# Performance work log

Hardware: AMD Instinct MI355X
Metric: run time of the kernel (lower is better)

## Reference

```python
import jax, jax.numpy as jnp
from jax import lax
import numpy as np

IN, G, H, L = 128, 5, 512, 256   # input_size, n_genres, hidden_dim, latent_dim
E = 2 * H                         # encoder_hidden_dim (bidirectional)
B, T = 128, 256
SLOPE = 0.01                      # torch LeakyReLU default


def _gru(xt, h, Wih, Whh, bih, bhh):
    # torch.nn.GRUCell: gates ordered r, z, n
    gi = xt @ Wih.T + bih         # [B, 3H]
    gh = h @ Whh.T + bhh          # [B, 3H]
    ir, iz, inn = jnp.split(gi, 3, axis=-1)
    hr, hz, hn = jnp.split(gh, 3, axis=-1)
    r = jax.nn.sigmoid(ir + hr)
    z = jax.nn.sigmoid(iz + hz)
    n = jnp.tanh(inn + r * hn)
    return (1.0 - z) * n + z * h


def _leaky(v):
    return jnp.where(v >= 0, v, SLOPE * v)


def setup_inputs() -> dict:
    key = jax.random.key(0)
    ks = jax.random.split(key, 32)
    it = iter(range(32))

    def p(shape, fan_in):
        s = 1.0 / np.sqrt(fan_in)
        return jax.random.uniform(ks[next(it)], shape, jnp.float32, -s, s)

    inp = {
        "x": jax.random.normal(ks[next(it)], (B, T, IN + G), jnp.float32),
        "latent_genre_vec": jax.random.uniform(ks[next(it)], (B, G), jnp.float32),
        "eps": jax.random.normal(ks[next(it)], (B, L - G), jnp.float32),
    }
    # forward encoder GRUCell (input IN+G -> H)
    inp["Wih_e"] = p((3 * H, IN + G), H); inp["Whh_e"] = p((3 * H, H), H)
    inp["bih_e"] = p((3 * H,), H);        inp["bhh_e"] = p((3 * H,), H)
    # backward encoder GRUCell
    inp["Wih_be"] = p((3 * H, IN + G), H); inp["Whh_be"] = p((3 * H, H), H)
    inp["bih_be"] = p((3 * H,), H);        inp["bhh_be"] = p((3 * H,), H)
    # decoder GRUCell (input IN -> H)
    inp["Wih_d"] = p((3 * H, IN), H); inp["Whh_d"] = p((3 * H, H), H)
    inp["bih_d"] = p((3 * H,), H);    inp["bhh_d"] = p((3 * H,), H)
    # fc_mu: [Linear(E,E)+LeakyReLU, Linear(E, L-G)]
    inp["W_mu0"] = p((E, E), E); inp["b_mu0"] = p((E,), E)
    inp["W_mu1"] = p((L - G, E), E); inp["b_mu1"] = p((L - G,), E)
    # fc_logvar
    inp["W_lv0"] = p((E, E), E); inp["b_lv0"] = p((E,), E)
    inp["W_lv1"] = p((L - G, E), E); inp["b_lv1"] = p((L - G,), E)
    # fc_latent: [Linear(L,L)+LeakyReLU, Linear(L, H)]
    inp["W_lat0"] = p((L, L), L); inp["b_lat0"] = p((L,), L)
    inp["W_lat1"] = p((H, L), L); inp["b_lat1"] = p((H,), L)
    # fc_decoder final Linear(H, IN) (fc_decoder[0] is dead code in the original loop)
    inp["W_dec1"] = p((IN, H), H); inp["b_dec1"] = p((IN,), H)
    return inp


def reference(x, latent_genre_vec, eps,
              Wih_e, Whh_e, bih_e, bhh_e,
              Wih_be, Whh_be, bih_be, bhh_be,
              Wih_d, Whh_d, bih_d, bhh_d,
              W_mu0, b_mu0, W_mu1, b_mu1,
              W_lv0, b_lv0, W_lv1, b_lv1,
              W_lat0, b_lat0, W_lat1, b_lat1,
              W_dec1, b_dec1):
    b = x.shape[0]
    xs = jnp.swapaxes(x, 0, 1)  # [T, B, IN+G]
    h0 = jnp.zeros((b, H), x.dtype)

    def enc_step(h, xt):
        return _gru(xt, h, Wih_e, Whh_e, bih_e, bhh_e), None

    def benc_step(h, xt):
        return _gru(xt, h, Wih_be, Whh_be, bih_be, bhh_be), None

    h_fwd, _ = lax.scan(enc_step, h0, xs)
    h_bwd, _ = lax.scan(benc_step, h0, xs, reverse=True)
    hidden = jnp.concatenate([h_fwd, h_bwd], axis=1)  # [B, 2H]

    mu = _leaky(hidden @ W_mu0.T + b_mu0) @ W_mu1.T + b_mu1        # [B, L-G]
    logvar = _leaky(hidden @ W_lv0.T + b_lv0) @ W_lv1.T + b_lv1    # [B, L-G]

    z = mu + jnp.exp(0.5 * logvar) * eps
    z = jnp.concatenate([z, latent_genre_vec], axis=1)             # [B, L]

    dec_h = _leaky(z @ W_lat0.T + b_lat0) @ W_lat1.T + b_lat1      # [B, H]

    note0 = x[:, 0, :IN]  # [B, IN]

    def dec_step(carry, _):
        h, note = carry
        h = _gru(note, h, Wih_d, Whh_d, bih_d, bhh_d)
        # faithful to original: final fc_decoder layer applied to hidden
        note = h @ W_dec1.T + b_dec1
        return (h, note), note

    _, notes = lax.scan(dec_step, (dec_h, note0), None, length=x.shape[1] - 1)
    output = jnp.concatenate([note0[:, None, :], jnp.swapaxes(notes, 0, 1)], axis=1)  # [B, T, IN]
    return output, mu, logvar
```

## Files before the change

### kernel.cpp

```cpp
#include <hip/hip_runtime.h>

#define B_ 128
#define T_ 256
#define IN_ 128
#define G_ 5
#define H_ 512
#define G3_ 1536
#define E_ 1024
#define L_ 256
#define LG_ 251
#define INPG_ 133

#define MU_OFF (B_*T_*IN_)
#define LV_OFF (MU_OFF + B_*LG_)

typedef __attribute__((ext_vector_type(8))) short bf16x8;
typedef __attribute__((ext_vector_type(4))) float f32x4;
typedef unsigned long long u64;

__device__ __forceinline__ float bf2f(unsigned short s) {
    return __uint_as_float(((unsigned)s) << 16);
}
__device__ __forceinline__ unsigned short f2bf(float f) {
    unsigned x = __float_as_uint(f);
    unsigned r = (x + 0x7fffu + ((x >> 16) & 1u)) >> 16;
    return (unsigned short)r;
}
__device__ __forceinline__ float sigf(float v) {
    return 1.f / (1.f + __expf(-v));
}
__device__ __forceinline__ int ld_flag(const int* p) {
    return __hip_atomic_load(p, __ATOMIC_RELAXED, __HIP_MEMORY_SCOPE_AGENT);
}
__device__ __forceinline__ void st_flag(int* p, int v) {
    __hip_atomic_store(p, v, __ATOMIC_RELAXED, __HIP_MEMORY_SCOPE_AGENT);
}
__device__ __forceinline__ u64 ld_h64(const void* p) {
    return __hip_atomic_load((const u64*)p, __ATOMIC_RELAXED, __HIP_MEMORY_SCOPE_AGENT);
}
__device__ __forceinline__ void st_h32(void* p, unsigned v) {
    __hip_atomic_store((unsigned*)p, v, __ATOMIC_RELAXED, __HIP_MEMORY_SCOPE_AGENT);
}


__global__ void xpad_k(const float* __restrict__ x, ushort* __restrict__ xb) {
    int id = blockIdx.x * 256 + threadIdx.x;
    if (id >= T_ * B_ * 160) return;
    int t = id / (B_ * 160);
    int rem = id - t * (B_ * 160);
    int b = rem / 160, c = rem - b * 160;
    float v = (c < INPG_) ? x[((size_t)b * T_ + t) * INPG_ + c] : 0.f;
    xb[id] = f2bf(v);
}

__global__ void pack_we(const float* __restrict__ Wih_f, const float* __restrict__ Whh_f,
                        const float* __restrict__ Wih_b, const float* __restrict__ Whh_b,
                        ushort* __restrict__ WE) {
    int id = blockIdx.x * 256 + threadIdx.x;
    int lane = id & 63;
    int rest = id >> 6;
    int ks = rest % 63;
    int cb = (rest / 63) & 31;
    int dir = rest / (63 * 32);
    if (dir >= 2) return;
    const float* Wih = dir ? Wih_b : Wih_f;
    const float* Whh = dir ? Whh_b : Whh_f;
    int n = lane & 15, kb = lane >> 4;
    int p, ksp;
    if (ks < 21)      { p = 0; ksp = ks; }
    else if (ks < 42) { p = 1; ksp = ks - 21; }
    else if (ks < 47) { p = 2; ksp = ks - 42; }
    else              { p = 3; ksp = ks - 47; }
    int j = cb * 16 + n;
    int row = (p == 0) ? j : (p == 1) ? 512 + j : 1024 + j;
    #pragma unroll
    for (int e = 0; e < 8; ++e) {
        int k = ksp * 32 + kb * 8 + e;
        float v;
        if (p == 3)      v = Whh[(size_t)row * 512 + k];
        else if (p == 2) v = (k < INPG_) ? Wih[(size_t)row * INPG_ + k] : 0.f;
        else v = (k < INPG_) ? Wih[(size_t)row * INPG_ + k]
               : (k < 160)   ? 0.f
               : Whh[(size_t)row * 512 + (k - 160)];
        WE[(size_t)id * 8 + e] = f2bf(v);
    }
}

__global__ void wfused_k(const float* __restrict__ Wih_d, const float* __restrict__ Wdec1,
                         float* __restrict__ Wf) {
    int id = blockIdx.x * 256 + threadIdx.x;
    if (id >= G3_ * H_) return;
    int r = id >> 9, c = id & 511;
    float s = 0.f;
    for (int m = 0; m < 128; ++m)
        s += Wih_d[(size_t)r * 128 + m] * Wdec1[(size_t)m * 512 + c];
    Wf[id] = s;
}

__global__ void bfi_k(const float* __restrict__ Wih_d, const float* __restrict__ b_dec1,
                      const float* __restrict__ bih_d, float* __restrict__ bfi) {
    int r = blockIdx.x * 256 + threadIdx.x;
    if (r >= G3_) return;
    float s = bih_d[r];
    for (int m = 0; m < 128; ++m)
        s += Wih_d[(size_t)r * 128 + m] * b_dec1[m];
    bfi[r] = s;
}

__global__ void pack_wd(const float* __restrict__ Wf, const float* __restrict__ Whh,
                        ushort* __restrict__ WD, int fused) {
    int id = blockIdx.x * 256 + threadIdx.x;
    int lane = id & 63;
    int rest = id >> 6;
    int ks = rest & 63;
    int cb = rest >> 6;
    if (cb >= 32) return;
    int p = ks >> 4, ksp = ks & 15;
    int n = lane & 15, kb = lane >> 4;
    int j = cb * 16 + n;
    int row = (p == 0) ? j : (p == 1) ? 512 + j : 1024 + j;
    #pragma unroll
    for (int e = 0; e < 8; ++e) {
        int k = ksp * 32 + kb * 8 + e;
        float v;
        if (p <= 1) v = fused ? (Wf[(size_t)row * 512 + k] + Whh[(size_t)row * 512 + k])
                              : Whh[(size_t)row * 512 + k];
        else if (p == 2) v = fused ? Wf[(size_t)row * 512 + k] : 0.f;
        else v = Whh[(size_t)row * 512 + k];
        WD[(size_t)id * 8 + e] = f2bf(v);
    }
}

__global__ void pack_wdec(const float* __restrict__ Wdec1, ushort* __restrict__ pk) {
    int id = blockIdx.x * 256 + threadIdx.x;
    if (id >= 8192) return;
    int lane = id & 63, ch = id >> 6;
    int nt = ch >> 4, ks = ch & 15;
    int n = nt * 16 + (lane & 15);
    int k0 = ks * 32 + (lane >> 4) * 8;
    #pragma unroll
    for (int e = 0; e < 8; ++e)
        pk[(size_t)id * 8 + e] = f2bf(Wdec1[(size_t)n * 512 + k0 + e]);
}

__global__ void zero_init(ushort* __restrict__ hb, int* __restrict__ ef,
                          int* __restrict__ df) {
    int id = blockIdx.x * 256 + threadIdx.x;
    if (id < 4 * 65536) hb[id] = 0;
    if (id < 4096) ef[id] = 0;
    if (id < 2048) df[id] = 0;
}

__global__ void note0_k2(const float* __restrict__ x, float* __restrict__ out,
                         float* __restrict__ note0f) {
    int id = blockIdx.x * 256 + threadIdx.x;
    if (id >= B_ * IN_) return;
    int b = id >> 7, n = id & 127;
    float v = x[((size_t)b * T_) * INPG_ + n];
    out[((size_t)b * T_) * IN_ + n] = v;
    note0f[(size_t)b * 128 + n] = v;
}

__global__ void cvt_h0(const float* __restrict__ src, ushort* __restrict__ dst) {
    int id = blockIdx.x * 256 + threadIdx.x;
    if (id < B_ * H_) dst[id] = f2bf(src[id]);
}

__global__ void tile_w(const float* __restrict__ W, ushort4* __restrict__ out,
                       int N, int K, int KC) {
    int id = blockIdx.x * 256 + threadIdx.x;
    if (id >= KC * N) return;
    int kc = id / N, n = id - kc * N;
    int k = kc * 4;
    ushort4 u;
    u.x = f2bf(k + 0 < K ? W[(size_t)n * K + k + 0] : 0.f);
    u.y = f2bf(k + 1 < K ? W[(size_t)n * K + k + 1] : 0.f);
    u.z = f2bf(k + 2 < K ? W[(size_t)n * K + k + 2] : 0.f);
    u.w = f2bf(k + 3 < K ? W[(size_t)n * K + k + 3] : 0.f);
    out[(size_t)kc * N + n] = u;
}

__global__ __launch_bounds__(256) void enc_persist(
    const ushort* __restrict__ xb16, const ushort* __restrict__ WE,
    ushort* __restrict__ hb,
    float* __restrict__ hidden,
    const float* __restrict__ bih_f, const float* __restrict__ bhh_f,
    const float* __restrict__ bih_b, const float* __restrict__ bhh_b,
    int* __restrict__ flags)
{
    __shared__ ushort As[32 * 680];
    __shared__ ushort Ws[63 * 512];
    __shared__ float gs[4][512];
    int bid = blockIdx.x;
    int dir = bid >> 7, bt = (bid >> 5) & 3, cb = bid & 31;
    int b0 = bt * 32;
    int tid = threadIdx.x;
    const float* bih = dir ? bih_b : bih_f;
    const float* bhh = dir ? bhh_b : bhh_f;

    {
        const ushort* src = WE + (size_t)((dir * 32 + cb) * 63) * 512;
        for (int c = tid; c < 4032; c += 256)
            *(uint4*)&Ws[c * 8] = *(const uint4*)&src[c * 8];
    }
    int bA = tid >> 3;
    int j0 = cb * 16 + 2 * (tid & 7), j1 = j0 + 1;
    float b_r0 = bih[j0] + bhh[j0],        b_r1 = bih[j1] + bhh[j1];
    float b_z0 = bih[512 + j0] + bhh[512 + j0], b_z1 = bih[512 + j1] + bhh[512 + j1];
    float b_in0 = bih[1024 + j0],          b_in1 = bih[1024 + j1];
    float b_hn0 = bhh[1024 + j0],          b_hn1 = bhh[1024 + j1];
    float hc0 = 0.f, hc1 = 0.f;

    int lane = tid & 63, wv = tid >> 6;
    int m = lane & 15, kb = lane >> 4;
    int nk  = (wv == 2) ? 5 : (wv == 3) ? 16 : 21;
    int ksb = (wv == 0) ? 0 : (wv == 1) ? 21 : (wv == 2) ? 42 : 47;
    int kcol0 = (wv == 3) ? 160 : 0;
    int ai0 = m * 680 + kcol0 + kb * 8;
    int ai1 = (16 + m) * 680 + kcol0 + kb * 8;
    const int* fpoll = &flags[((bid & ~31) + (lane & 31)) * 16];

    auto stage_x = [&](int t2) {
        int tt2 = dir ? (255 - t2) : t2;
        const ushort* xr2 = xb16 + (size_t)tt2 * (B_ * 160);
        #pragma unroll
        for (int i = 0; i < 3; ++i) {
            int c = tid + i * 256;
            if (c < 640) {
                int row = c / 20, off = c - row * 20;
                *(uint4*)((char*)As + row * 1360 + off * 16) =
                    *(const uint4*)(xr2 + (size_t)(b0 + row) * 160 + off * 8);
            }
        }
    };
    stage_x(0);

    for (int t = 0; t < T_; ++t) {
        int pp = t & 1;
        const ushort* hin = hb + (size_t)(pp * 2 + dir) * 65536;
        ushort* hout = hb + (size_t)((pp ^ 1) * 2 + dir) * 65536;
        if (t > 0) {
            if (wv == 0)
                while (!__all(ld_flag(fpoll) >= t)) __builtin_amdgcn_s_sleep(1);
            __syncthreads();
        }
        {
            u64 vb[16];
            #pragma unroll
            for (int i = 0; i < 16; ++i) {
                int c = tid + i * 256;
                int row = c >> 7, off = c & 127;
                vb[i] = ld_h64(hin + (size_t)(b0 + row) * 512 + off * 4);
            }
            #pragma unroll
            for (int i = 0; i < 16; ++i) {
                int c = tid + i * 256;
                int row = c >> 7, off = c & 127;
                *(u64*)((char*)As + row * 1360 + 320 + off * 8) = vb[i];
            }
        }
        __syncthreads();
        f32x4 acc0 = {0.f,0.f,0.f,0.f}, acc1 = {0.f,0.f,0.f,0.f};
        const ushort* Bp = &Ws[ksb * 512 + lane * 8];
        for (int ks = 0; ks < nk; ++ks) {
            bf16x8 bfr = *(const bf16x8*)(Bp + (size_t)ks * 512);
            bf16x8 a0 = *(const bf16x8*)&As[ai0 + ks * 32];
            bf16x8 a1 = *(const bf16x8*)&As[ai1 + ks * 32];
            acc0 = __builtin_amdgcn_mfma_f32_16x16x32_bf16(a0, bfr, acc0, 0, 0, 0);
            acc1 = __builtin_amdgcn_mfma_f32_16x16x32_bf16(a1, bfr, acc1, 0, 0, 0);
        }
        #pragma unroll
        for (int i = 0; i < 4; ++i) {
            gs[wv][(kb * 4 + i) * 16 + m] = acc0[i];
            gs[wv][(16 + kb * 4 + i) * 16 + m] = acc1[i];
        }
        __syncthreads();
        {
            int o0 = 2 * tid, o1 = o0 + 1;
            float r0 = sigf(gs[0][o0] + b_r0);
            float z0 = sigf(gs[1][o0] + b_z0);
            float n0 = tanhf(gs[2][o0] + b_in0 + r0 * (gs[3][o0] + b_hn0));
            hc0 = (1.f - z0) * n0 + z0 * hc0;
            float r1 = sigf(gs[0][o1] + b_r1);
            float z1 = sigf(gs[1][o1] + b_z1);
            float n1 = tanhf(gs[2][o1] + b_in1 + r1 * (gs[3][o1] + b_hn1));
            hc1 = (1.f - z1) * n1 + z1 * hc1;
            unsigned pkd = (unsigned)f2bf(hc0) | ((unsigned)f2bf(hc1) << 16);
            st_h32((char*)hout + ((size_t)(b0 + bA) * 512 + j0) * 2, pkd);
            if (t == 255) {
                float2 hv = {hc0, hc1};
                *(float2*)&hidden[(size_t)(b0 + bA) * 1024 + dir * 512 + j0] = hv;
            }
        }
        __syncthreads();
        if (t < 255) {
            if (tid == 0) st_flag(&flags[bid * 16], t + 1);
            stage_x(t + 1);
        }
    }
}

__global__ __launch_bounds__(256) void dec_persist(
    const ushort* __restrict__ hdec0, const ushort* __restrict__ WD2,
    const ushort* __restrict__ WD1, ushort* __restrict__ hist,
    const float* __restrict__ h0f, const float* __restrict__ bfi,
    const float* __restrict__ bhh, const float* __restrict__ gi0,
    int* __restrict__ flags)
{
    __shared__ ushort As[32 * 520];
    __shared__ ushort Ws[64 * 512];
    __shared__ float gs[4][512];
    int bid = blockIdx.x;
    int bt = bid >> 5, cb = bid & 31;
    int b0 = bt * 32, tid = threadIdx.x;
    {
        const ushort* src = WD2 + (size_t)(cb * 64) * 512;
        for (int c = tid; c < 4096; c += 256)
            *(uint4*)&Ws[c * 8] = *(const uint4*)&src[c * 8];
    }
    int bA = tid >> 3;
    int j0 = cb * 16 + 2 * (tid & 7), j1 = j0 + 1;
    float f_r0 = bfi[j0] + bhh[j0],             f_r1 = bfi[j1] + bhh[j1];
    float f_z0 = bfi[512 + j0] + bhh[512 + j0], f_z1 = bfi[512 + j1] + bhh[512 + j1];
    float f_in0 = bfi[1024 + j0],               f_in1 = bfi[1024 + j1];
    float f_hn0 = bhh[1024 + j0],               f_hn1 = bhh[1024 + j1];
    float bh_r0 = bhh[j0], bh_r1 = bhh[j1];
    float bh_z0 = bhh[512 + j0], bh_z1 = bhh[512 + j1];
    float hc0 = h0f[(size_t)(b0 + bA) * 512 + j0];
    float hc1 = h0f[(size_t)(b0 + bA) * 512 + j1];
    float g0r = gi0[(size_t)(b0 + bA) * G3_ + j0];
    float g1r = gi0[(size_t)(b0 + bA) * G3_ + j1];
    float g0z = gi0[(size_t)(b0 + bA) * G3_ + 512 + j0];
    float g1z = gi0[(size_t)(b0 + bA) * G3_ + 512 + j1];
    float g0n = gi0[(size_t)(b0 + bA) * G3_ + 1024 + j0];
    float g1n = gi0[(size_t)(b0 + bA) * G3_ + 1024 + j1];

    int lane = tid & 63, wv = tid >> 6;
    int m = lane & 15, kb = lane >> 4;
    int ai0 = m * 520 + kb * 8, ai1 = (16 + m) * 520 + kb * 8;
    const ushort* WD1s = WD1 + (size_t)(cb * 64 + wv * 16) * 512 + lane * 8;
    const int* fpoll = &flags[((bid & ~31) + (lane & 31)) * 16];

    for (int t = 1; t < T_; ++t) {
        if (t >= 2) {
            if (wv == 0)
                while (!__all(ld_flag(fpoll) >= t - 1)) __builtin_amdgcn_s_sleep(1);
            __syncthreads();
        }
        const ushort* hsrc = (t == 1) ? hdec0 : hist + (size_t)(t - 2) * 65536;
        {
            u64 vb[16];
            #pragma unroll
            for (int i = 0; i < 16; ++i) {
                int c = tid + i * 256;
                int row = c >> 7, off = c & 127;
                vb[i] = ld_h64(hsrc + (size_t)(b0 + row) * 512 + off * 4);
            }
            #pragma unroll
            for (int i = 0; i < 16; ++i) {
                int c = tid + i * 256;
                int row = c >> 7, off = c & 127;
                *(u64*)((char*)As + row * 1040 + off * 8) = vb[i];
            }
        }
        __syncthreads();
        f32x4 acc0 = {0.f,0.f,0.f,0.f}, acc1 = {0.f,0.f,0.f,0.f};
        if (t == 1) {
            if (wv != 2) {
                for (int ks = 0; ks < 16; ++ks) {
                    bf16x8 bfr = *(const bf16x8*)(WD1s + (size_t)ks * 512);
                    bf16x8 a0 = *(const bf16x8*)&As[ai0 + ks * 32];
                    bf16x8 a1 = *(const bf16x8*)&As[ai1 + ks * 32];
                    acc0 = __builtin_amdgcn_mfma_f32_16x16x32_bf16(a0, bfr, acc0, 0, 0, 0);
                    acc1 = __builtin_amdgcn_mfma_f32_16x16x32_bf16(a1, bfr, acc1, 0, 0, 0);
                }
            }
        } else {
            const ushort* Bp = &Ws[(wv * 16) * 512 + lane * 8];
            for (int ks = 0; ks < 16; ++ks) {
                bf16x8 bfr = *(const bf16x8*)(Bp + (size_t)ks * 512);
                bf16x8 a0 = *(const bf16x8*)&As[ai0 + ks * 32];
                bf16x8 a1 = *(const bf16x8*)&As[ai1 + ks * 32];
                acc0 = __builtin_amdgcn_mfma_f32_16x16x32_bf16(a0, bfr, acc0, 0, 0, 0);
                acc1 = __builtin_amdgcn_mfma_f32_16x16x32_bf16(a1, bfr, acc1, 0, 0, 0);
            }
        }
        #pragma unroll
        for (int i = 0; i < 4; ++i) {
            gs[wv][(kb * 4 + i) * 16 + m] = acc0[i];
            gs[wv][(16 + kb * 4 + i) * 16 + m] = acc1[i];
        }
        __syncthreads();
        {
            int o0 = 2 * tid, o1 = o0 + 1;
            float r0, z0, n0, r1, z1, n1;
            if (t == 1) {
                r0 = sigf(gs[0][o0] + g0r + bh_r0);
                z0 = sigf(gs[1][o0] + g0z + bh_z0);
                n0 = tanhf(gs[2][o0] + g0n + r0 * (gs[3][o0] + f_hn0));
                r1 = sigf(gs[0][o1] + g1r + bh_r1);
                z1 = sigf(gs[1][o1] + g1z + bh_z1);
                n1 = tanhf(gs[2][o1] + g1n + r1 * (gs[3][o1] + f_hn1));
            } else {
                r0 = sigf(gs[0][o0] + f_r0);
                z0 = sigf(gs[1][o0] + f_z0);
                n0 = tanhf(gs[2][o0] + f_in0 + r0 * (gs[3][o0] + f_hn0));
                r1 = sigf(gs[0][o1] + f_r1);
                z1 = sigf(gs[1][o1] + f_z1);
                n1 = tanhf(gs[2][o1] + f_in1 + r1 * (gs[3][o1] + f_hn1));
            }
            hc0 = (1.f - z0) * n0 + z0 * hc0;
            hc1 = (1.f - z1) * n1 + z1 * hc1;
            unsigned pkd = (unsigned)f2bf(hc0) | ((unsigned)f2bf(hc1) << 16);
            st_h32((char*)(hist + (size_t)(t - 1) * 65536) +
                   ((size_t)(b0 + bA) * 512 + j0) * 2, pkd);
        }
        __syncthreads();
        if (t < 255 && tid == 0) st_flag(&flags[bid * 16], t);
    }
}

__global__ __launch_bounds__(256) void notes_mfma(
    const ushort* __restrict__ hist, const ushort* __restrict__ pk,
    const float* __restrict__ bd, float* __restrict__ out)
{
    __shared__ ushort hs[32 * 520];
    int m0 = blockIdx.x * 32;
    int tid = threadIdx.x;
    #pragma unroll
    for (int i = 0; i < 8; ++i) {
        int c = tid + i * 256;
        int row = c >> 6, off = c & 63;
        *(uint4*)((char*)hs + row * 1040 + off * 16) =
            *(const uint4*)(hist + (size_t)(m0 + row) * 512 + off * 8);
    }
    __syncthreads();
    int lane = tid & 63, wv = tid >> 6;
    int m = lane & 15, kb = lane >> 4;
    int nt0 = wv * 2;
    f32x4 acc00 = {0.f,0.f,0.f,0.f}, acc01 = {0.f,0.f,0.f,0.f};
    f32x4 acc10 = {0.f,0.f,0.f,0.f}, acc11 = {0.f,0.f,0.f,0.f};
    for (int ks = 0; ks < 16; ++ks) {
        bf16x8 a0 = *(const bf16x8*)&hs[m * 520 + ks * 32 + kb * 8];
        bf16x8 a1 = *(const bf16x8*)&hs[(16 + m) * 520 + ks * 32 + kb * 8];
        bf16x8 bf0 = *(const bf16x8*)&pk[(size_t)((nt0 * 16 + ks) * 64 + lane) * 8];
        bf16x8 bf1 = *(const bf16x8*)&pk[(size_t)(((nt0 + 1) * 16 + ks) * 64 + lane) * 8];
        acc00 = __builtin_amdgcn_mfma_f32_16x16x32_bf16(a0, bf0, acc00, 0, 0, 0);
        acc01 = __builtin_amdgcn_mfma_f32_16x16x32_bf16(a0, bf1, acc01, 0, 0, 0);
        acc10 = __builtin_amdgcn_mfma_f32_16x16x32_bf16(a1, bf0, acc10, 0, 0, 0);
        acc11 = __builtin_amdgcn_mfma_f32_16x16x32_bf16(a1, bf1, acc11, 0, 0, 0);
    }
    int n0 = nt0 * 16 + (lane & 15), n1 = (nt0 + 1) * 16 + (lane & 15);
    #pragma unroll
    for (int i = 0; i < 4; ++i) {
        int r0 = m0 + kb * 4 + i;
        int r1 = r0 + 16;
        int t0 = r0 >> 7, b0r = r0 & 127;
        int t1 = r1 >> 7, b1r = r1 & 127;
        out[((size_t)b0r * T_ + (t0 + 1)) * IN_ + n0] = acc00[i] + bd[n0];
        out[((size_t)b0r * T_ + (t0 + 1)) * IN_ + n1] = acc01[i] + bd[n1];
        out[((size_t)b1r * T_ + (t1 + 1)) * IN_ + n0] = acc10[i] + bd[n0];
        out[((size_t)b1r * T_ + (t1 + 1)) * IN_ + n1] = acc11[i] + bd[n1];
    }
}

__global__ __launch_bounds__(256) void gemm_t4(
    const float* __restrict__ A, const ushort4* __restrict__ Wt,
    const float* __restrict__ bias, float* __restrict__ C,
    int M, int N, int K, int act)
{
    int nb = blockIdx.x, mb = blockIdx.y;
    int tid = threadIdx.x;
    int n = nb * 64 + (tid & 63);
    int mq = tid >> 6;
    int m0 = mb * 32;
    __shared__ float Asm[32][36];
    float acc[8];
    #pragma unroll
    for (int i = 0; i < 8; ++i) acc[i] = 0.f;
    for (int k0 = 0; k0 < K; k0 += 32) {
        int r = tid >> 3, c = (tid & 7) << 2;
        float4 v = *(const float4*)&A[(size_t)(m0 + r) * K + k0 + c];
        Asm[r][c] = v.x; Asm[r][c+1] = v.y; Asm[r][c+2] = v.z; Asm[r][c+3] = v.w;
        __syncthreads();
        #pragma unroll
        for (int kc = 0; kc < 8; ++kc) {
            float w0 = 0.f, w1 = 0.f, w2 = 0.f, w3 = 0.f;
            if (n < N) {
                ushort4 u = Wt[(size_t)((k0 >> 2) + kc) * N + n];
                w0 = bf2f(u.x); w1 = bf2f(u.y); w2 = bf2f(u.z); w3 = bf2f(u.w);
            }
            #pragma unroll
            for (int i = 0; i < 8; ++i) {
                int mm = mq * 8 + i;
                acc[i] += Asm[mm][kc*4+0]*w0 + Asm[mm][kc*4+1]*w1
                        + Asm[mm][kc*4+2]*w2 + Asm[mm][kc*4+3]*w3;
            }
        }
        __syncthreads();
    }
    if (n < N) {
        #pragma unroll
        for (int i = 0; i < 8; ++i) {
            int mm = m0 + mq * 8 + i;
            float v = acc[i] + bias[n];
            if (act == 1) v = (v >= 0.f) ? v : 0.01f * v;
            C[(size_t)mm * N + n] = v;
        }
    }
}

__global__ void z_k(const float* __restrict__ out, const float* __restrict__ eps,
                    const float* __restrict__ genre, float* __restrict__ zc) {
    int id = blockIdx.x * 256 + threadIdx.x;
    if (id >= B_ * L_) return;
    int b = id >> 8, c = id & 255;
    float v;
    if (c < LG_) {
        float mu = out[MU_OFF + (size_t)b * LG_ + c];
        float lv = out[LV_OFF + (size_t)b * LG_ + c];
        v = mu + expf(0.5f * lv) * eps[(size_t)b * LG_ + c];
    } else {
        v = genre[(size_t)b * G_ + (c - LG_)];
    }
    zc[id] = v;
}

extern "C" void kernel_launch(void* const* d_in, const int* in_sizes, int n_in,
                              void* d_out, int out_size, void* d_ws, size_t ws_size,
                              hipStream_t stream) {
    (void)in_sizes; (void)n_in; (void)out_size; (void)ws_size;
    const float* x      = (const float*)d_in[0];
    const float* genre  = (const float*)d_in[1];
    const float* eps    = (const float*)d_in[2];
    const float* Wih_e  = (const float*)d_in[3];
    const float* Whh_e  = (const float*)d_in[4];
    const float* bih_e  = (const float*)d_in[5];
    const float* bhh_e  = (const float*)d_in[6];
    const float* Wih_be = (const float*)d_in[7];
    const float* Whh_be = (const float*)d_in[8];
    const float* bih_be = (const float*)d_in[9];
    const float* bhh_be = (const float*)d_in[10];
    const float* Wih_d  = (const float*)d_in[11];
    const float* Whh_d  = (const float*)d_in[12];
    const float* bih_d  = (const float*)d_in[13];
    const float* bhh_d  = (const float*)d_in[14];
    const float* W_mu0  = (const float*)d_in[15];
    const float* b_mu0  = (const float*)d_in[16];
    const float* W_mu1  = (const float*)d_in[17];
    const float* b_mu1  = (const float*)d_in[18];
    const float* W_lv0  = (const float*)d_in[19];
    const float* b_lv0  = (const float*)d_in[20];
    const float* W_lv1  = (const float*)d_in[21];
    const float* b_lv1  = (const float*)d_in[22];
    const float* W_lat0 = (const float*)d_in[23];
    const float* b_lat0 = (const float*)d_in[24];
    const float* W_lat1 = (const float*)d_in[25];
    const float* b_lat1 = (const float*)d_in[26];
    const float* W_dec1 = (const float*)d_in[27];
    const float* b_dec1 = (const float*)d_in[28];
    float* out = (float*)d_out;

    char* ws = (char*)d_ws;
    size_t off = 0;
    auto alloc = [&](size_t bytes) -> char* {
        char* p = ws + off;
        off = (off + bytes + 255) & ~(size_t)255;
        return p;
    };
    ushort* xb16  = (ushort*)alloc((size_t)T_ * B_ * 160 * 2);
    ushort* WE    = (ushort*)alloc((size_t)2 * 32 * 63 * 512 * 2);
    ushort* WD2   = (ushort*)alloc((size_t)32 * 64 * 512 * 2);
    ushort* WD1   = (ushort*)alloc((size_t)32 * 64 * 512 * 2);
    float*  Wf    = (float*)alloc((size_t)G3_ * H_ * 4);
    float*  bfi   = (float*)alloc(G3_ * 4);
    ushort* hb_e  = (ushort*)alloc((size_t)4 * 65536 * 2);
    ushort* hist  = (ushort*)alloc((size_t)255 * 65536 * 2);
    ushort* hdec0 = (ushort*)alloc((size_t)65536 * 2);
    ushort* pkdec = (ushort*)alloc((size_t)8192 * 8 * 2);
    int*    eflag = (int*)alloc((size_t)4096 * 4);
    int*    dflag = (int*)alloc((size_t)2048 * 4);
    float*  note0f= (float*)alloc((size_t)B_ * 128 * 4);
    float*  gi0   = (float*)alloc((size_t)B_ * G3_ * 4);
    float*  hidden= (float*)alloc((size_t)B_ * E_ * 4);
    float*  t0buf = (float*)alloc((size_t)B_ * E_ * 4);
    float*  t1buf = (float*)alloc((size_t)B_ * E_ * 4);
    float*  zcbuf = (float*)alloc((size_t)B_ * L_ * 4);
    float*  t2buf = (float*)alloc((size_t)B_ * L_ * 4);
    float*  t3buf = (float*)alloc((size_t)B_ * H_ * 4);

    ushort4* T_Wmu0  = (ushort4*)alloc((size_t)256 * E_ * 8);
    ushort4* T_Wmu1  = (ushort4*)alloc((size_t)256 * LG_ * 8);
    ushort4* T_Wlv0  = (ushort4*)alloc((size_t)256 * E_ * 8);
    ushort4* T_Wlv1  = (ushort4*)alloc((size_t)256 * LG_ * 8);
    ushort4* T_Wlat0 = (ushort4*)alloc((size_t)64 * L_ * 8);
    ushort4* T_Wlat1 = (ushort4*)alloc((size_t)64 * H_ * 8);
    ushort4* T_Wihd  = (ushort4*)alloc((size_t)32 * G3_ * 8);

    xpad_k<<<(T_ * B_ * 160 + 255) / 256, 256, 0, stream>>>(x, xb16);
    pack_we<<<1008, 256, 0, stream>>>(Wih_e, Whh_e, Wih_be, Whh_be, WE);
    wfused_k<<<(G3_ * H_ + 255) / 256, 256, 0, stream>>>(Wih_d, W_dec1, Wf);
    bfi_k<<<6, 256, 0, stream>>>(Wih_d, b_dec1, bih_d, bfi);
    pack_wd<<<512, 256, 0, stream>>>(Wf, Whh_d, WD2, 1);
    pack_wd<<<512, 256, 0, stream>>>(Wf, Whh_d, WD1, 0);
    pack_wdec<<<32, 256, 0, stream>>>(W_dec1, pkdec);
    zero_init<<<1024, 256, 0, stream>>>(hb_e, eflag, dflag);
    note0_k2<<<(B_ * IN_ + 255) / 256, 256, 0, stream>>>(x, out, note0f);

    auto tile = [&](const float* W, ushort4* dst, int N, int K) {
        int KC = (K + 3) / 4;
        tile_w<<<(KC * N + 255) / 256, 256, 0, stream>>>(W, dst, N, K, KC);
    };
    tile(W_mu0,  T_Wmu0,  E_,  E_);
    tile(W_mu1,  T_Wmu1,  LG_, E_);
    tile(W_lv0,  T_Wlv0,  E_,  E_);
    tile(W_lv1,  T_Wlv1,  LG_, E_);
    tile(W_lat0, T_Wlat0, L_,  L_);
    tile(W_lat1, T_Wlat1, H_,  L_);
    tile(Wih_d,  T_Wihd,  G3_, IN_);

    enc_persist<<<256, 256, 0, stream>>>(xb16, WE, hb_e, hidden,
                                         bih_e, bhh_e, bih_be, bhh_be, eflag);

    {
        dim3 g1(16, 4), g2(4, 4), g3(4, 4), g4(8, 4), g5(24, 4);
        gemm_t4<<<g1, 256, 0, stream>>>(hidden, T_Wmu0, b_mu0, t0buf, B_, E_, E_, 1);
        gemm_t4<<<g2, 256, 0, stream>>>(t0buf, T_Wmu1, b_mu1, out + MU_OFF, B_, LG_, E_, 0);
        gemm_t4<<<g1, 256, 0, stream>>>(hidden, T_Wlv0, b_lv0, t1buf, B_, E_, E_, 1);
        gemm_t4<<<g2, 256, 0, stream>>>(t1buf, T_Wlv1, b_lv1, out + LV_OFF, B_, LG_, E_, 0);
        z_k<<<(B_ * L_ + 255) / 256, 256, 0, stream>>>(out, eps, genre, zcbuf);
        gemm_t4<<<g3, 256, 0, stream>>>(zcbuf, T_Wlat0, b_lat0, t2buf, B_, L_, L_, 1);
        gemm_t4<<<g4, 256, 0, stream>>>(t2buf, T_Wlat1, b_lat1, t3buf, B_, H_, L_, 0);
        gemm_t4<<<g5, 256, 0, stream>>>(note0f, T_Wihd, bih_d, gi0, B_, G3_, IN_, 0);
    }
    cvt_h0<<<(B_ * H_ + 255) / 256, 256, 0, stream>>>(t3buf, hdec0);

    dec_persist<<<128, 256, 0, stream>>>(hdec0, WD2, WD1, hist, t3buf,
                                         bfi, bhh_d, gi0, dflag);

    notes_mfma<<<1020, 256, 0, stream>>>(hist, pkdec, b_dec1, out);
}
```

Baseline: 2.303 ms.

## Keep GRU weights in registers and compute all gates per wave in persistent RNN kernels

The encoder and decoder persistent kernels now run 128 threads per block, with each wave holding its slice of the r, z and n gate weights in VGPRs instead of LDS. Each wave computes all four gate accumulators for 16 batch rows, which removes the shared-memory gate exchange and two block barriers per timestep. Readiness flags are now per wave (two per block, polled as one 64-bit load), and hidden state is stored as 16-bit elements. Fast rcp-based sigmoid and tanh are also added. The risks are heavy register pressure from about 63 bf16x8 weight vectors per thread, and the use of approximate transcendentals.

```diff
diff --git a/kernel.cpp b/kernel.cpp
--- a/kernel.cpp
+++ b/kernel.cpp
@@ -27,7 +27,12 @@
     return (unsigned short)r;
 }
 __device__ __forceinline__ float sigf(float v) {
-    return 1.f / (1.f + __expf(-v));
+    return __builtin_amdgcn_rcpf(1.f + __expf(-v));
+}
+__device__ __forceinline__ float ftanh(float x) {
+    x = fminf(15.f, fmaxf(-15.f, x));
+    float e = __expf(2.f * x);
+    return (e - 1.f) * __builtin_amdgcn_rcpf(e + 1.f);
 }
 __device__ __forceinline__ int ld_flag(const int* p) {
     return __hip_atomic_load(p, __ATOMIC_RELAXED, __HIP_MEMORY_SCOPE_AGENT);
@@ -38,8 +43,11 @@
 __device__ __forceinline__ u64 ld_h64(const void* p) {
     return __hip_atomic_load((const u64*)p, __ATOMIC_RELAXED, __HIP_MEMORY_SCOPE_AGENT);
 }
-__device__ __forceinline__ void st_h32(void* p, unsigned v) {
-    __hip_atomic_store((unsigned*)p, v, __ATOMIC_RELAXED, __HIP_MEMORY_SCOPE_AGENT);
+__device__ __forceinline__ u64 ld_f64(const void* p) {
+    return __hip_atomic_load((const u64*)p, __ATOMIC_RELAXED, __HIP_MEMORY_SCOPE_AGENT);
+}
+__device__ __forceinline__ void st_h16(ushort* p, ushort v) {
+    __hip_atomic_store(p, v, __ATOMIC_RELAXED, __HIP_MEMORY_SCOPE_AGENT);
 }
 
 
@@ -143,10 +151,8 @@
         pk[(size_t)id * 8 + e] = f2bf(Wdec1[(size_t)n * 512 + k0 + e]);
 }
 
-__global__ void zero_init(ushort* __restrict__ hb, int* __restrict__ ef,
-                          int* __restrict__ df) {
-    int id = blockIdx.x * 256 + threadIdx.x;
-    if (id < 4 * 65536) hb[id] = 0;
+__global__ void zero_init(int* __restrict__ ef, int* __restrict__ df) {
+    int id = blockIdx.x * 256 + threadIdx.x;
     if (id < 4096) ef[id] = 0;
     if (id < 2048) df[id] = 0;
 }
@@ -180,7 +186,9 @@
     out[(size_t)kc * N + n] = u;
 }
 
-__global__ __launch_bounds__(256) void enc_persist(
+#define MFMA16(a, b, c) __builtin_amdgcn_mfma_f32_16x16x32_bf16((a), (b), (c), 0, 0, 0)
+
+__global__ __launch_bounds__(128) void enc_persist(
     const ushort* __restrict__ xb16, const ushort* __restrict__ WE,
     ushort* __restrict__ hb,
     float* __restrict__ hidden,
@@ -188,235 +196,236 @@
     const float* __restrict__ bih_b, const float* __restrict__ bhh_b,
     int* __restrict__ flags)
 {
-    __shared__ ushort As[32 * 680];
-    __shared__ ushort Ws[63 * 512];
-    __shared__ float gs[4][512];
+    __shared__ ushort As[52000];
     int bid = blockIdx.x;
     int dir = bid >> 7, bt = (bid >> 5) & 3, cb = bid & 31;
+    int gb = dir * 4 + bt;
     int b0 = bt * 32;
     int tid = threadIdx.x;
+    int lane = tid & 63, wv = tid >> 6;
     const float* bih = dir ? bih_b : bih_f;
     const float* bhh = dir ? bhh_b : bhh_f;
 
+    int m = lane & 15, kb = lane >> 4;
+    int j = cb * 16 + m;
+    int rowbase = wv * 16;
+    int rb = b0 + rowbase + ((lane >> 4) << 2);
+
+    bf16x8 wR[21], wZ[21], wNx[5], wNh[16];
     {
-        const ushort* src = WE + (size_t)((dir * 32 + cb) * 63) * 512;
-        for (int c = tid; c < 4032; c += 256)
-            *(uint4*)&Ws[c * 8] = *(const uint4*)&src[c * 8];
-    }
-    int bA = tid >> 3;
-    int j0 = cb * 16 + 2 * (tid & 7), j1 = j0 + 1;
-    float b_r0 = bih[j0] + bhh[j0],        b_r1 = bih[j1] + bhh[j1];
-    float b_z0 = bih[512 + j0] + bhh[512 + j0], b_z1 = bih[512 + j1] + bhh[512 + j1];
-    float b_in0 = bih[1024 + j0],          b_in1 = bih[1024 + j1];
-    float b_hn0 = bhh[1024 + j0],          b_hn1 = bhh[1024 + j1];
-    float hc0 = 0.f, hc1 = 0.f;
-
-    int lane = tid & 63, wv = tid >> 6;
-    int m = lane & 15, kb = lane >> 4;
-    int nk  = (wv == 2) ? 5 : (wv == 3) ? 16 : 21;
-    int ksb = (wv == 0) ? 0 : (wv == 1) ? 21 : (wv == 2) ? 42 : 47;
-    int kcol0 = (wv == 3) ? 160 : 0;
-    int ai0 = m * 680 + kcol0 + kb * 8;
-    int ai1 = (16 + m) * 680 + kcol0 + kb * 8;
-    const int* fpoll = &flags[((bid & ~31) + (lane & 31)) * 16];
-
-    auto stage_x = [&](int t2) {
-        int tt2 = dir ? (255 - t2) : t2;
-        const ushort* xr2 = xb16 + (size_t)tt2 * (B_ * 160);
-        #pragma unroll
-        for (int i = 0; i < 3; ++i) {
-            int c = tid + i * 256;
-            if (c < 640) {
-                int row = c / 20, off = c - row * 20;
-                *(uint4*)((char*)As + row * 1360 + off * 16) =
-                    *(const uint4*)(xr2 + (size_t)(b0 + row) * 160 + off * 8);
-            }
-        }
-    };
-    stage_x(0);
+        const ushort* ws = WE + (size_t)((dir * 32 + cb) * 63) * 512 + lane * 8;
+        #pragma unroll
+        for (int k = 0; k < 21; ++k) wR[k] = *(const bf16x8*)(ws + (size_t)k * 512);
+        #pragma unroll
+        for (int k = 0; k < 21; ++k) wZ[k] = *(const bf16x8*)(ws + (size_t)(21 + k) * 512);
+        #pragma unroll
+        for (int k = 0; k < 5; ++k)  wNx[k] = *(const bf16x8*)(ws + (size_t)(42 + k) * 512);
+        #pragma unroll
+        for (int k = 0; k < 16; ++k) wNh[k] = *(const bf16x8*)(ws + (size_t)(47 + k) * 512);
+    }
+    float b_r = bih[j] + bhh[j];
+    float b_z = bih[512 + j] + bhh[512 + j];
+    float b_in = bih[1024 + j];
+    float b_hn = bhh[1024 + j];
+    float hc[4] = {0.f, 0.f, 0.f, 0.f};
+    int ab = (rowbase + m) * 680 + kb * 8;
+    const u64* fp = (const u64*)&flags[(gb * 32 + wv * 16 + m) * 2];
+
+    for (int c = tid; c < 4096; c += 128) {
+        int row = c >> 7, off = c & 127;
+        *(u64*)((char*)As + row * 1360 + 320 + off * 8) = 0ull;
+    }
+    {
+        const ushort* xr = xb16 + (size_t)(dir ? 255 : 0) * (B_ * 160);
+        #pragma unroll
+        for (int i = 0; i < 5; ++i) {
+            int c = tid + i * 128;
+            int row = c / 20, off = c - row * 20;
+            *(uint4*)((char*)As + row * 1360 + off * 16) =
+                *(const uint4*)(xr + (size_t)(b0 + row) * 160 + off * 8);
+        }
+    }
 
     for (int t = 0; t < T_; ++t) {
         int pp = t & 1;
         const ushort* hin = hb + (size_t)(pp * 2 + dir) * 65536;
         ushort* hout = hb + (size_t)((pp ^ 1) * 2 + dir) * 65536;
         if (t > 0) {
-            if (wv == 0)
-                while (!__all(ld_flag(fpoll) >= t)) __builtin_amdgcn_s_sleep(1);
+            for (;;) {
+                u64 v = __hip_atomic_load(fp, __ATOMIC_RELAXED, __HIP_MEMORY_SCOPE_AGENT);
+                bool ok = ((unsigned)v >= (unsigned)t) && ((unsigned)(v >> 32) >= (unsigned)t);
+                if (__all(ok)) break;
+                __builtin_amdgcn_s_sleep(1);
+            }
+            const ushort* hsv = hin + (size_t)b0 * 512 + wv * 256;
+            u64 vb[16];
+            #pragma unroll
+            for (int k = 0; k < 16; ++k)
+                vb[k] = ld_h64(hsv + (size_t)k * 512 + lane * 4);
+            #pragma unroll
+            for (int k = 0; k < 16; ++k) {
+                *(u64*)((char*)As + k * 1360 + 320 + (wv * 64 + lane) * 8) = vb[k];
+                vb[k] = ld_h64(hsv + (size_t)(k + 16) * 512 + lane * 4);
+            }
+            #pragma unroll
+            for (int k = 0; k < 16; ++k)
+                *(u64*)((char*)As + (k + 16) * 1360 + 320 + (wv * 64 + lane) * 8) = vb[k];
+        }
+        __syncthreads();
+        f32x4 aR = {0.f,0.f,0.f,0.f}, aZ = {0.f,0.f,0.f,0.f};
+        f32x4 aNx = {0.f,0.f,0.f,0.f}, aNh = {0.f,0.f,0.f,0.f};
+        #pragma unroll
+        for (int ks = 0; ks < 21; ++ks) {
+            bf16x8 a = *(const bf16x8*)&As[ab + ks * 32];
+            aR = MFMA16(a, wR[ks], aR);
+            aZ = MFMA16(a, wZ[ks], aZ);
+            if (ks < 5) aNx = MFMA16(a, wNx[ks], aNx);
+            if (ks < 16) {
+                bf16x8 ah = *(const bf16x8*)&As[ab + 160 + ks * 32];
+                aNh = MFMA16(ah, wNh[ks], aNh);
+            }
+        }
+        #pragma unroll
+        for (int i = 0; i < 4; ++i) {
+            float r = sigf(aR[i] + b_r);
+            float z = sigf(aZ[i] + b_z);
+            float n = ftanh(aNx[i] + b_in + r * (aNh[i] + b_hn));
+            hc[i] = (1.f - z) * n + z * hc[i];
+            st_h16(hout + (size_t)(rb + i) * 512 + j, f2bf(hc[i]));
+        }
+        if (t == 255) {
+            #pragma unroll
+            for (int i = 0; i < 4; ++i)
+                hidden[(size_t)(rb + i) * 1024 + dir * 512 + j] = hc[i];
+        } else {
+            asm volatile("s_waitcnt vmcnt(0)" ::: "memory");
+            if (lane == 0)
+                st_flag(&flags[(gb * 32 + cb) * 2 + wv], t + 1);
             __syncthreads();
-        }
-        {
-            u64 vb[16];
-            #pragma unroll
-            for (int i = 0; i < 16; ++i) {
-                int c = tid + i * 256;
-                int row = c >> 7, off = c & 127;
-                vb[i] = ld_h64(hin + (size_t)(b0 + row) * 512 + off * 4);
-            }
-            #pragma unroll
-            for (int i = 0; i < 16; ++i) {
-                int c = tid + i * 256;
-                int row = c >> 7, off = c & 127;
-                *(u64*)((char*)As + row * 1360 + 320 + off * 8) = vb[i];
-            }
-        }
-        __syncthreads();
-        f32x4 acc0 = {0.f,0.f,0.f,0.f}, acc1 = {0.f,0.f,0.f,0.f};
-        const ushort* Bp = &Ws[ksb * 512 + lane * 8];
-        for (int ks = 0; ks < nk; ++ks) {
-            bf16x8 bfr = *(const bf16x8*)(Bp + (size_t)ks * 512);
-            bf16x8 a0 = *(const bf16x8*)&As[ai0 + ks * 32];
-            bf16x8 a1 = *(const bf16x8*)&As[ai1 + ks * 32];
-            acc0 = __builtin_amdgcn_mfma_f32_16x16x32_bf16(a0, bfr, acc0, 0, 0, 0);
-            acc1 = __builtin_amdgcn_mfma_f32_16x16x32_bf16(a1, bfr, acc1, 0, 0, 0);
-        }
-        #pragma unroll
-        for (int i = 0; i < 4; ++i) {
-            gs[wv][(kb * 4 + i) * 16 + m] = acc0[i];
-            gs[wv][(16 + kb * 4 + i) * 16 + m] = acc1[i];
-        }
-        __syncthreads();
-        {
-            int o0 = 2 * tid, o1 = o0 + 1;
-            float r0 = sigf(gs[0][o0] + b_r0);
-            float z0 = sigf(gs[1][o0] + b_z0);
-            float n0 = tanhf(gs[2][o0] + b_in0 + r0 * (gs[3][o0] + b_hn0));
-            hc0 = (1.f - z0) * n0 + z0 * hc0;
-            float r1 = sigf(gs[0][o1] + b_r1);
-            float z1 = sigf(gs[1][o1] + b_z1);
-            float n1 = tanhf(gs[2][o1] + b_in1 + r1 * (gs[3][o1] + b_hn1));
-            hc1 = (1.f - z1) * n1 + z1 * hc1;
-            unsigned pkd = (unsigned)f2bf(hc0) | ((unsigned)f2bf(hc1) << 16);
-            st_h32((char*)hout + ((size_t)(b0 + bA) * 512 + j0) * 2, pkd);
-            if (t == 255) {
-                float2 hv = {hc0, hc1};
-                *(float2*)&hidden[(size_t)(b0 + bA) * 1024 + dir * 512 + j0] = hv;
-            }
-        }
-        __syncthreads();
-        if (t < 255) {
-            if (tid == 0) st_flag(&flags[bid * 16], t + 1);
-            stage_x(t + 1);
-        }
-    }
-}
-
-__global__ __launch_bounds__(256) void dec_persist(
+            int tt2 = dir ? (254 - t) : (t + 1);
+            const ushort* xr2 = xb16 + (size_t)tt2 * (B_ * 160);
+            #pragma unroll
+            for (int i2 = 0; i2 < 5; ++i2) {
+                int c = tid + i2 * 128;
+                int row = c / 20, off2 = c - row * 20;
+                *(uint4*)((char*)As + row * 1360 + off2 * 16) =
+                    *(const uint4*)(xr2 + (size_t)(b0 + row) * 160 + off2 * 8);
+            }
+        }
+    }
+}
+
+__global__ __launch_bounds__(128) void dec_persist(
     const ushort* __restrict__ hdec0, const ushort* __restrict__ WD2,
     const ushort* __restrict__ WD1, ushort* __restrict__ hist,
     const float* __restrict__ h0f, const float* __restrict__ bfi,
     const float* __restrict__ bhh, const float* __restrict__ gi0,
     int* __restrict__ flags)
 {
-    __shared__ ushort As[32 * 520];
-    __shared__ ushort Ws[64 * 512];
-    __shared__ float gs[4][512];
+    __shared__ ushort As[52000];
     int bid = blockIdx.x;
     int bt = bid >> 5, cb = bid & 31;
     int b0 = bt * 32, tid = threadIdx.x;
-    {
-        const ushort* src = WD2 + (size_t)(cb * 64) * 512;
-        for (int c = tid; c < 4096; c += 256)
-            *(uint4*)&Ws[c * 8] = *(const uint4*)&src[c * 8];
-    }
-    int bA = tid >> 3;
-    int j0 = cb * 16 + 2 * (tid & 7), j1 = j0 + 1;
-    float f_r0 = bfi[j0] + bhh[j0],             f_r1 = bfi[j1] + bhh[j1];
-    float f_z0 = bfi[512 + j0] + bhh[512 + j0], f_z1 = bfi[512 + j1] + bhh[512 + j1];
-    float f_in0 = bfi[1024 + j0],               f_in1 = bfi[1024 + j1];
-    float f_hn0 = bhh[1024 + j0],               f_hn1 = bhh[1024 + j1];
-    float bh_r0 = bhh[j0], bh_r1 = bhh[j1];
-    float bh_z0 = bhh[512 + j0], bh_z1 = bhh[512 + j1];
-    float hc0 = h0f[(size_t)(b0 + bA) * 512 + j0];
-    float hc1 = h0f[(size_t)(b0 + bA) * 512 + j1];
-    float g0r = gi0[(size_t)(b0 + bA) * G3_ + j0];
-    float g1r = gi0[(size_t)(b0 + bA) * G3_ + j1];
-    float g0z = gi0[(size_t)(b0 + bA) * G3_ + 512 + j0];
-    float g1z = gi0[(size_t)(b0 + bA) * G3_ + 512 + j1];
-    float g0n = gi0[(size_t)(b0 + bA) * G3_ + 1024 + j0];
-    float g1n = gi0[(size_t)(b0 + bA) * G3_ + 1024 + j1];
-
     int lane = tid & 63, wv = tid >> 6;
     int m = lane & 15, kb = lane >> 4;
-    int ai0 = m * 520 + kb * 8, ai1 = (16 + m) * 520 + kb * 8;
-    const ushort* WD1s = WD1 + (size_t)(cb * 64 + wv * 16) * 512 + lane * 8;
-    const int* fpoll = &flags[((bid & ~31) + (lane & 31)) * 16];
+    int j = cb * 16 + m;
+    int rowbase = wv * 16;
+    int rb = b0 + rowbase + ((lane >> 4) << 2);
+
+    bf16x8 wR[16], wZ[16], wGi[16], wGh[16];
+    {
+        const ushort* ws = WD2 + (size_t)(cb * 64) * 512 + lane * 8;
+        #pragma unroll
+        for (int k = 0; k < 16; ++k) wR[k] = *(const bf16x8*)(ws + (size_t)k * 512);
+        #pragma unroll
+        for (int k = 0; k < 16; ++k) wZ[k] = *(const bf16x8*)(ws + (size_t)(16 + k) * 512);
+        #pragma unroll
+        for (int k = 0; k < 16; ++k) wGi[k] = *(const bf16x8*)(ws + (size_t)(32 + k) * 512);
+        #pragma unroll
+        for (int k = 0; k < 16; ++k) wGh[k] = *(const bf16x8*)(ws + (size_t)(48 + k) * 512);
+    }
+    float f_r = bfi[j] + bhh[j];
+    float f_z = bfi[512 + j] + bhh[512 + j];
+    float f_in = bfi[1024 + j];
+    float f_hn = bhh[1024 + j];
+    float bh_r = bhh[j], bh_z = bhh[512 + j];
+    float hc[4], g_r[4], g_z[4], g_n[4];
+    #pragma unroll
+    for (int i = 0; i < 4; ++i) {
+        hc[i]  = h0f[(size_t)(rb + i) * 512 + j];
+        g_r[i] = gi0[(size_t)(rb + i) * G3_ + j];
+        g_z[i] = gi0[(size_t)(rb + i) * G3_ + 512 + j];
+        g_n[i] = gi0[(size_t)(rb + i) * G3_ + 1024 + j];
+    }
+    int ab = (rowbase + m) * 520 + kb * 8;
+    const u64* fp = (const u64*)&flags[(bt * 32 + wv * 16 + m) * 2];
 
     for (int t = 1; t < T_; ++t) {
+        const ushort* hsrc = (t == 1) ? hdec0 : hist + (size_t)(t - 2) * 65536;
         if (t >= 2) {
-            if (wv == 0)
-                while (!__all(ld_flag(fpoll) >= t - 1)) __builtin_amdgcn_s_sleep(1);
+            int need = t - 1;
+            for (;;) {
+                u64 v = __hip_atomic_load(fp, __ATOMIC_RELAXED, __HIP_MEMORY_SCOPE_AGENT);
+                bool ok = ((unsigned)v >= (unsigned)need) && ((unsigned)(v >> 32) >= (unsigned)need);
+                if (__all(ok)) break;
+                __builtin_amdgcn_s_sleep(1);
+            }
+        }
+        {
+            const ushort* hsv = hsrc + (size_t)b0 * 512 + wv * 256;
+            u64 vb[16];
+            #pragma unroll
+            for (int k = 0; k < 16; ++k)
+                vb[k] = ld_h64(hsv + (size_t)k * 512 + lane * 4);
+            #pragma unroll
+            for (int k = 0; k < 16; ++k) {
+                *(u64*)((char*)As + k * 1040 + (wv * 64 + lane) * 8) = vb[k];
+                vb[k] = ld_h64(hsv + (size_t)(k + 16) * 512 + lane * 4);
+            }
+            #pragma unroll
+            for (int k = 0; k < 16; ++k)
+                *(u64*)((char*)As + (k + 16) * 1040 + (wv * 64 + lane) * 8) = vb[k];
+        }
+        __syncthreads();
+        f32x4 aR = {0.f,0.f,0.f,0.f}, aZ = {0.f,0.f,0.f,0.f};
+        f32x4 aGi = {0.f,0.f,0.f,0.f}, aGh = {0.f,0.f,0.f,0.f};
+        if (t == 1) {
+            const ushort* w1 = WD1 + (size_t)(cb * 64) * 512 + lane * 8;
+            #pragma unroll
+            for (int ks = 0; ks < 16; ++ks) {
+                bf16x8 a = *(const bf16x8*)&As[ab + ks * 32];
+                aR = MFMA16(a, *(const bf16x8*)(w1 + (size_t)ks * 512), aR);
+                aZ = MFMA16(a, *(const bf16x8*)(w1 + (size_t)(16 + ks) * 512), aZ);
+                aGh = MFMA16(a, *(const bf16x8*)(w1 + (size_t)(48 + ks) * 512), aGh);
+            }
+        } else {
+            #pragma unroll
+            for (int ks = 0; ks < 16; ++ks) {
+                bf16x8 a = *(const bf16x8*)&As[ab + ks * 32];
+                aR = MFMA16(a, wR[ks], aR);
+                aZ = MFMA16(a, wZ[ks], aZ);
+                aGi = MFMA16(a, wGi[ks], aGi);
+                aGh = MFMA16(a, wGh[ks], aGh);
+            }
+        }
+        ushort* hdst = hist + (size_t)(t - 1) * 65536;
+        #pragma unroll
+        for (int i = 0; i < 4; ++i) {
+            float cr = (t == 1) ? (g_r[i] + bh_r) : f_r;
+            float cz = (t == 1) ? (g_z[i] + bh_z) : f_z;
+            float cn = (t == 1) ? g_n[i] : f_in;
+            float r = sigf(aR[i] + cr);
+            float z = sigf(aZ[i] + cz);
+            float n = ftanh(aGi[i] + cn + r * (aGh[i] + f_hn));
+            hc[i] = (1.f - z) * n + z * hc[i];
+            st_h16(hdst + (size_t)(rb + i) * 512 + j, f2bf(hc[i]));
+        }
+        if (t < 255) {
+            asm volatile("s_waitcnt vmcnt(0)" ::: "memory");
+            if (lane == 0)
+                st_flag(&flags[(bt * 32 + cb) * 2 + wv], t);
             __syncthreads();
         }
-        const ushort* hsrc = (t == 1) ? hdec0 : hist + (size_t)(t - 2) * 65536;
-        {
-            u64 vb[16];
-            #pragma unroll
-            for (int i = 0; i < 16; ++i) {
-                int c = tid + i * 256;
-                int row = c >> 7, off = c & 127;
-                vb[i] = ld_h64(hsrc + (size_t)(b0 + row) * 512 + off * 4);
-            }
-            #pragma unroll
-            for (int i = 0; i < 16; ++i) {
-                int c = tid + i * 256;
-                int row = c >> 7, off = c & 127;
-                *(u64*)((char*)As + row * 1040 + off * 8) = vb[i];
-            }
-        }
-        __syncthreads();
-        f32x4 acc0 = {0.f,0.f,0.f,0.f}, acc1 = {0.f,0.f,0.f,0.f};
-        if (t == 1) {
-            if (wv != 2) {
-                for (int ks = 0; ks < 16; ++ks) {
-                    bf16x8 bfr = *(const bf16x8*)(WD1s + (size_t)ks * 512);
-                    bf16x8 a0 = *(const bf16x8*)&As[ai0 + ks * 32];
-                    bf16x8 a1 = *(const bf16x8*)&As[ai1 + ks * 32];
-                    acc0 = __builtin_amdgcn_mfma_f32_16x16x32_bf16(a0, bfr, acc0, 0, 0, 0);
-                    acc1 = __builtin_amdgcn_mfma_f32_16x16x32_bf16(a1, bfr, acc1, 0, 0, 0);
-                }
-            }
-        } else {
-            const ushort* Bp = &Ws[(wv * 16) * 512 + lane * 8];
-            for (int ks = 0; ks < 16; ++ks) {
-                bf16x8 bfr = *(const bf16x8*)(Bp + (size_t)ks * 512);
-                bf16x8 a0 = *(const bf16x8*)&As[ai0 + ks * 32];
-                bf16x8 a1 = *(const bf16x8*)&As[ai1 + ks * 32];
-                acc0 = __builtin_amdgcn_mfma_f32_16x16x32_bf16(a0, bfr, acc0, 0, 0, 0);
-                acc1 = __builtin_amdgcn_mfma_f32_16x16x32_bf16(a1, bfr, acc1, 0, 0, 0);
-            }
-        }
-        #pragma unroll
-        for (int i = 0; i < 4; ++i) {
-            gs[wv][(kb * 4 + i) * 16 + m] = acc0[i];
-            gs[wv][(16 + kb * 4 + i) * 16 + m] = acc1[i];
-        }
-        __syncthreads();
-        {
-            int o0 = 2 * tid, o1 = o0 + 1;
-            float r0, z0, n0, r1, z1, n1;
-            if (t == 1) {
-                r0 = sigf(gs[0][o0] + g0r + bh_r0);
-                z0 = sigf(gs[1][o0] + g0z + bh_z0);
-                n0 = tanhf(gs[2][o0] + g0n + r0 * (gs[3][o0] + f_hn0));
-                r1 = sigf(gs[0][o1] + g1r + bh_r1);
-                z1 = sigf(gs[1][o1] + g1z + bh_z1);
-                n1 = tanhf(gs[2][o1] + g1n + r1 * (gs[3][o1] + f_hn1));
-            } else {
-                r0 = sigf(gs[0][o0] + f_r0);
-                z0 = sigf(gs[1][o0] + f_z0);
-                n0 = tanhf(gs[2][o0] + f_in0 + r0 * (gs[3][o0] + f_hn0));
-                r1 = sigf(gs[0][o1] + f_r1);
-                z1 = sigf(gs[1][o1] + f_z1);
-                n1 = tanhf(gs[2][o1] + f_in1 + r1 * (gs[3][o1] + f_hn1));
-            }
-            hc0 = (1.f - z0) * n0 + z0 * hc0;
-            hc1 = (1.f - z1) * n1 + z1 * hc1;
-            unsigned pkd = (unsigned)f2bf(hc0) | ((unsigned)f2bf(hc1) << 16);
-            st_h32((char*)(hist + (size_t)(t - 1) * 65536) +
-                   ((size_t)(b0 + bA) * 512 + j0) * 2, pkd);
-        }
-        __syncthreads();
-        if (t < 255 && tid == 0) st_flag(&flags[bid * 16], t);
     }
 }
 
@@ -445,10 +454,10 @@
         bf16x8 a1 = *(const bf16x8*)&hs[(16 + m) * 520 + ks * 32 + kb * 8];
         bf16x8 bf0 = *(const bf16x8*)&pk[(size_t)((nt0 * 16 + ks) * 64 + lane) * 8];
         bf16x8 bf1 = *(const bf16x8*)&pk[(size_t)(((nt0 + 1) * 16 + ks) * 64 + lane) * 8];
-        acc00 = __builtin_amdgcn_mfma_f32_16x16x32_bf16(a0, bf0, acc00, 0, 0, 0);
-        acc01 = __builtin_amdgcn_mfma_f32_16x16x32_bf16(a0, bf1, acc01, 0, 0, 0);
-        acc10 = __builtin_amdgcn_mfma_f32_16x16x32_bf16(a1, bf0, acc10, 0, 0, 0);
-        acc11 = __builtin_amdgcn_mfma_f32_16x16x32_bf16(a1, bf1, acc11, 0, 0, 0);
+        acc00 = MFMA16(a0, bf0, acc00);
+        acc01 = MFMA16(a0, bf1, acc01);
+        acc10 = MFMA16(a1, bf0, acc10);
+        acc11 = MFMA16(a1, bf1, acc11);
     }
     int n0 = nt0 * 16 + (lane & 15), n1 = (nt0 + 1) * 16 + (lane & 15);
     #pragma unroll
@@ -604,7 +613,7 @@
     pack_wd<<<512, 256, 0, stream>>>(Wf, Whh_d, WD2, 1);
     pack_wd<<<512, 256, 0, stream>>>(Wf, Whh_d, WD1, 0);
     pack_wdec<<<32, 256, 0, stream>>>(W_dec1, pkdec);
-    zero_init<<<1024, 256, 0, stream>>>(hb_e, eflag, dflag);
+    zero_init<<<16, 256, 0, stream>>>(eflag, dflag);
     note0_k2<<<(B_ * IN_ + 255) / 256, 256, 0, stream>>>(x, out, note0f);
 
     auto tile = [&](const float* W, ushort4* dst, int N, int K) {
@@ -619,7 +628,7 @@
     tile(W_lat1, T_Wlat1, H_,  L_);
     tile(Wih_d,  T_Wihd,  G3_, IN_);
 
-    enc_persist<<<256, 256, 0, stream>>>(xb16, WE, hb_e, hidden,
+    enc_persist<<<256, 128, 0, stream>>>(xb16, WE, hb_e, hidden,
                                          bih_e, bhh_e, bih_be, bhh_be, eflag);
 
     {
@@ -635,7 +644,7 @@
     }
     cvt_h0<<<(B_ * H_ + 255) / 256, 256, 0, stream>>>(t3buf, hdec0);
 
-    dec_persist<<<128, 256, 0, stream>>>(hdec0, WD2, WD1, hist, t3buf,
+    dec_persist<<<128, 128, 0, stream>>>(hdec0, WD2, WD1, hist, t3buf,
                                          bfi, bhh_d, gi0, dflag);
 
     notes_mfma<<<1020, 256, 0, stream>>>(hist, pkdec, b_dec1, out);
```

Result: slower. 2.716 ms (+17.9%).
